# Kernel tuning notes

Measured on AMD Instinct MI355X. Metric: run time of the kernel, lower is better.

Reference implementation:

```python
import jax, jax.numpy as jnp
import numpy as np
from jax import lax

# Model hyperparameters (from module source: D_state=2, Expand=1; mamba-ssm defaults)
B_, C_, H_, W_ = 16, 128, 96, 96
D_MODEL = C_
D_INNER = 1 * D_MODEL          # expand = 1
D_STATE = 2
DT_RANK = (D_MODEL + 15) // 16  # ceil(d_model/16) = 8
D_CONV = 4
OUT_C = 128
LN_EPS = 1e-5


def setup_inputs() -> dict:
    key = jax.random.key(0)
    ks = jax.random.split(key, 10)
    s = 0.02
    x = jax.random.normal(ks[0], (B_, C_, H_, W_), dtype=jnp.float32)
    in_proj_w = jax.random.normal(ks[1], (2 * D_INNER, D_MODEL), dtype=jnp.float32) * s
    conv_w = jax.random.normal(ks[2], (D_INNER, 1, D_CONV), dtype=jnp.float32) * s
    conv_b = jnp.zeros((D_INNER,), dtype=jnp.float32)
    x_proj_w = jax.random.normal(ks[3], (DT_RANK + 2 * D_STATE, D_INNER), dtype=jnp.float32) * s
    dt_proj_w = jax.random.normal(ks[4], (D_INNER, DT_RANK), dtype=jnp.float32) * s
    # softplus^{-1}(0.01) so initial dt ~ 0.01 (standard mamba init)
    dt_proj_b = jnp.full((D_INNER,), float(np.log(np.expm1(0.01))), dtype=jnp.float32)
    A_log = jnp.log(jnp.broadcast_to(jnp.arange(1, D_STATE + 1, dtype=jnp.float32), (D_INNER, D_STATE)))
    D_param = jnp.ones((D_INNER,), dtype=jnp.float32)
    out_proj_w = jax.random.normal(ks[5], (OUT_C, D_INNER), dtype=jnp.float32) * s
    ln_gamma = jnp.ones((OUT_C,), dtype=jnp.float32)
    ln_beta = jnp.zeros((OUT_C,), dtype=jnp.float32)
    return {
        "x": x, "in_proj_w": in_proj_w, "conv_w": conv_w, "conv_b": conv_b,
        "x_proj_w": x_proj_w, "dt_proj_w": dt_proj_w, "dt_proj_b": dt_proj_b,
        "A_log": A_log, "D_param": D_param, "out_proj_w": out_proj_w,
        "ln_gamma": ln_gamma, "ln_beta": ln_beta,
    }


def _ssm_cha(x, in_proj_w, conv_w, conv_b, x_proj_w, dt_proj_w, dt_proj_b,
             A_log, D_param, out_proj_w, ln_gamma, ln_beta):
    b, c, h, w = x.shape
    L = h * w
    tokens = x.transpose(0, 2, 3, 1).reshape(b, L, c)  # [b, L, d_model]

    # in_proj -> (x_in, z)
    xz = jnp.einsum("bld,ed->ble", tokens, in_proj_w)  # [b, L, 2*d_inner]
    x_in, z = jnp.split(xz, 2, axis=-1)

    # causal depthwise conv1d over L, then SiLU
    xc = x_in.transpose(0, 2, 1)  # [b, d_inner, L]
    xc = lax.conv_general_dilated(
        xc, conv_w, window_strides=(1,), padding=[(D_CONV - 1, 0)],
        dimension_numbers=("NCH", "OIH", "NCH"), feature_group_count=D_INNER,
    ) + conv_b[None, :, None]
    x_in = jax.nn.silu(xc).transpose(0, 2, 1)  # [b, L, d_inner]

    # x_proj -> (dt, B, C)
    x_dbl = jnp.einsum("bld,ed->ble", x_in, x_proj_w)
    dt = x_dbl[..., :DT_RANK]
    Bc = x_dbl[..., DT_RANK:DT_RANK + D_STATE]         # [b, L, n]
    Cc = x_dbl[..., DT_RANK + D_STATE:]                # [b, L, n]
    dt = jax.nn.softplus(jnp.einsum("blr,dr->bld", dt, dt_proj_w) + dt_proj_b)

    # selective scan (diagonal A) via associative scan over L
    A = -jnp.exp(A_log)                                # [d_inner, n]
    dA = jnp.exp(dt[..., None] * A)                    # [b, L, d_inner, n]
    dBx = dt[..., None] * Bc[:, :, None, :] * x_in[..., None]

    def combine(e1, e2):
        a1, b1 = e1
        a2, b2 = e2
        return a1 * a2, a2 * b1 + b2

    _, hstate = lax.associative_scan(combine, (dA, dBx), axis=1)  # [b, L, d, n]
    y = jnp.sum(hstate * Cc[:, :, None, :], axis=-1) + D_param * x_in  # [b, L, d]

    y = y * jax.nn.silu(z)
    out = jnp.einsum("bld,od->blo", y, out_proj_w)     # [b, L, out_c]

    # LayerNorm over out_c
    mu = jnp.mean(out, axis=-1, keepdims=True)
    var = jnp.mean(jnp.square(out - mu), axis=-1, keepdims=True)
    out = (out - mu) * lax.rsqrt(var + LN_EPS) * ln_gamma + ln_beta

    return out.reshape(b, h, w, OUT_C).transpose(0, 3, 1, 2)


def reference(x, in_proj_w, conv_w, conv_b, x_proj_w, dt_proj_w, dt_proj_b,
              A_log, D_param, out_proj_w, ln_gamma, ln_beta):
    return _ssm_cha(x, in_proj_w, conv_w, conv_b, x_proj_w, dt_proj_w, dt_proj_b,
                    A_log, D_param, out_proj_w, ln_gamma, ln_beta)
```

## Files before the change

kernel.cpp:

```cpp
#include <hip/hip_runtime.h>
#include <hip/hip_bf16.h>

#define B_N 16
#define L_N 9216
#define LT64 144

typedef __attribute__((ext_vector_type(8))) short short8;
typedef __attribute__((ext_vector_type(4))) float floatx4;

__device__ __forceinline__ float bfu(unsigned short u) {
  return __uint_as_float(((unsigned int)u) << 16);
}
__device__ __forceinline__ unsigned short fbf(float f) {
  __hip_bfloat16 h = __float2bfloat16(f);
  return *(unsigned short*)&h;
}

__global__ __launch_bounds__(256) void k_prep(const float* __restrict__ w1,
                                              const float* __restrict__ w2,
                                              __hip_bfloat16* __restrict__ w1bt,
                                              __hip_bfloat16* __restrict__ w2bt) {
  int i = blockIdx.x * 256 + threadIdx.x;
  if (i < 256 * 128) w1bt[i] = __float2bfloat16(w1[i]);
  if (i < 128 * 128) w2bt[i] = __float2bfloat16(w2[i]);
}

__global__ __launch_bounds__(512, 4) void k_inproj_conv(
    const float* __restrict__ x, const __hip_bfloat16* __restrict__ w1bt,
    const float* __restrict__ cw, const float* __restrict__ cb,
    const float* __restrict__ xpw,
    __hip_bfloat16* __restrict__ xinb, __hip_bfloat16* __restrict__ zb,
    float* __restrict__ xdblT) {
  __shared__ __align__(16) char smem1[16384];
  __shared__ __align__(16) char smem2[34816];
  unsigned short* xs = (unsigned short*)smem1;
  unsigned short* xe = (unsigned short*)smem2;
  float (*cvs)[68] = (float(*)[68])smem2;
  float (*red)[12][64] = (float(*)[12][64])smem2;

  int blk = blockIdx.x, b = blk / LT64, lt = blk % LT64, l0 = lt * 64;
  int t = threadIdx.x;
  int lane = t & 63, wv = t >> 6;
  int col = lane & 15, quad = lane >> 4;

  const float* xb = x + (size_t)b * 128 * L_N + l0 - 16;
#pragma unroll
  for (int i = 0; i < 5; ++i) {
    int idx = t + i * 512;
    int c = idx & 127, q = idx >> 7;
    float4 v = {0.f, 0.f, 0.f, 0.f};
    if (!(lt == 0 && q < 4)) v = *(const float4*)(xb + (size_t)c * L_N + q * 4);
    int ch = c >> 3, ce = c & 7;
    if (q < 4) {
#pragma unroll
      for (int j = 0; j < 4; ++j) {
        int l = q * 4 + j;
        xe[l * 128 + (((ch ^ (l & 7)) << 3) | ce)] = fbf(((const float*)&v)[j]);
      }
    } else {
#pragma unroll
      for (int j = 0; j < 4; ++j) {
        int l = q * 4 - 16 + j;
        xs[l * 128 + (((ch ^ (l & 7)) << 3) | ce)] = fbf(((const float*)&v)[j]);
      }
    }
  }

  int e0 = wv * 32;
  const __hip_bfloat16* wbp = w1bt + (size_t)(e0 + col) * 128 + quad * 8;
  floatx4 vzero = {0.f, 0.f, 0.f, 0.f};
  floatx4 acc[2][5];
#pragma unroll
  for (int mi = 0; mi < 2; ++mi)
#pragma unroll
    for (int ni = 0; ni < 5; ++ni) acc[mi][ni] = vzero;
  short8 a0 = *(const short8*)(wbp);
  short8 a1 = *(const short8*)(wbp + 16 * 128);
  __syncthreads();

#pragma unroll
  for (int ks = 0; ks < 4; ++ks) {
    short8 n0, n1;
    if (ks < 3) {
      n0 = *(const short8*)(wbp + (ks + 1) * 32);
      n1 = *(const short8*)(wbp + 16 * 128 + (ks + 1) * 32);
    }
    short8 bfr[5];
    bfr[0] = *(const short8*)&xe[col * 128 + (((ks * 4 + quad) ^ (col & 7)) << 3)];
#pragma unroll
    for (int ni = 1; ni < 5; ++ni) {
      int row = (ni - 1) * 16 + col;
      bfr[ni] = *(const short8*)&xs[row * 128 + (((ks * 4 + quad) ^ (row & 7)) << 3)];
    }
#pragma unroll
    for (int ni = 0; ni < 5; ++ni) {
      acc[0][ni] = __builtin_amdgcn_mfma_f32_16x16x32_bf16(a0, bfr[ni], acc[0][ni], 0, 0, 0);
      acc[1][ni] = __builtin_amdgcn_mfma_f32_16x16x32_bf16(a1, bfr[ni], acc[1][ni], 0, 0, 0);
    }
    a0 = n0; a1 = n1;
  }
  __syncthreads();

  if (wv >= 4) {
    __hip_bfloat16* zbase = zb + ((size_t)b * 128 + (e0 - 128)) * L_N + l0;
#pragma unroll
    for (int mi = 0; mi < 2; ++mi)
#pragma unroll
      for (int r = 0; r < 4; ++r) {
        int dr = mi * 16 + quad * 4 + r;
#pragma unroll
        for (int ni = 1; ni < 5; ++ni)
          zbase[(size_t)dr * L_N + (ni - 1) * 16 + col] = __float2bfloat16(acc[mi][ni][r]);
      }
  } else {
#pragma unroll
    for (int mi = 0; mi < 2; ++mi)
#pragma unroll
      for (int r = 0; r < 4; ++r) {
        int d = e0 + mi * 16 + quad * 4 + r;
        if (col >= 13) cvs[d][col - 13] = acc[mi][0][r];
#pragma unroll
        for (int ni = 1; ni < 5; ++ni) cvs[d][3 + (ni - 1) * 16 + col] = acc[mi][ni][r];
      }
  }
  __syncthreads();

  float part[12];
#pragma unroll
  for (int m = 0; m < 12; ++m) part[m] = 0.f;
  for (int dd = 0; dd < 16; ++dd) {
    int d = wv * 16 + dd;
    float v = cb[d] + cw[d * 4 + 0] * cvs[d][lane] + cw[d * 4 + 1] * cvs[d][lane + 1]
                    + cw[d * 4 + 2] * cvs[d][lane + 2] + cw[d * 4 + 3] * cvs[d][lane + 3];
    v = v / (1.f + __expf(-v));
    xinb[((size_t)b * 128 + d) * L_N + l0 + lane] = __float2bfloat16(v);
#pragma unroll
    for (int m = 0; m < 12; ++m) part[m] += xpw[m * 128 + d] * v;
  }
  __syncthreads();
#pragma unroll
  for (int m = 0; m < 12; ++m) red[wv][m][lane] = part[m];
  __syncthreads();
  for (int idx = t; idx < 12 * 64; idx += 512) {
    int m = idx >> 6, l = idx & 63;
    float s = 0.f;
#pragma unroll
    for (int w8 = 0; w8 < 8; ++w8) s += red[w8][m][l];
    xdblT[((size_t)b * 12 + m) * L_N + l0 + l] = s;
  }
}

__global__ __launch_bounds__(256) void k_scan(
    const float* __restrict__ xdblT, const float* __restrict__ dtw,
    const float* __restrict__ dtb, const float* __restrict__ alog,
    const float* __restrict__ dpar,
    const __hip_bfloat16* __restrict__ xinb, const __hip_bfloat16* __restrict__ zb,
    __hip_bfloat16* __restrict__ yb) {
  __shared__ float agg[2][4][4];
  __shared__ float carry[2][2];
  int blk = blockIdx.x, b = blk >> 7, d = blk & 127;
  int t = threadIdx.x, lane = t & 63, wv = t >> 6;
  float A0 = -__expf(alog[2 * d]), A1 = -__expf(alog[2 * d + 1]);
  float Dv = dpar[d], dtbv = dtb[d];
  float w[8];
#pragma unroll
  for (int i = 0; i < 8; ++i) w[i] = dtw[d * 8 + i];
  if (t == 0) { carry[0][0] = 0.f; carry[0][1] = 0.f; }
  __syncthreads();
  const float* xdT = xdblT + (size_t)b * 12 * L_N;
  const unsigned short* xi = (const unsigned short*)xinb + ((size_t)b * 128 + d) * L_N;
  const unsigned short* zr = (const unsigned short*)zb + ((size_t)b * 128 + d) * L_N;
  unsigned short* yo = (unsigned short*)yb + ((size_t)b * 128 + d) * L_N;
  for (int it = 0; it < 9; ++it) {
    int p = it & 1;
    int lb = it * 1024 + t * 4;
    float4 q[12];
#pragma unroll
    for (int m = 0; m < 12; ++m) q[m] = *(const float4*)(xdT + (size_t)m * L_N + lb);
    ushort4 xu = *(const ushort4*)(xi + lb);
    ushort4 zu = *(const ushort4*)(zr + lb);
    float xv[4] = {bfu(xu.x), bfu(xu.y), bfu(xu.z), bfu(xu.w)};
    float zv[4] = {bfu(zu.x), bfu(zu.y), bfu(zu.z), bfu(zu.w)};
    float A0p[4], X0p[4], A1p[4], X1p[4];
#pragma unroll
    for (int j = 0; j < 4; ++j) {
      float dtp = dtbv;
#pragma unroll
      for (int m = 0; m < 8; ++m) dtp += w[m] * ((const float*)&q[m])[j];
      float dt = (dtp > 15.f) ? dtp : __logf(1.f + __expf(dtp));
      float a0 = __expf(dt * A0), a1 = __expf(dt * A1);
      float dtx = dt * xv[j];
      float x0 = dtx * ((const float*)&q[8])[j];
      float x1 = dtx * ((const float*)&q[9])[j];
      if (j == 0) { A0p[0] = a0; X0p[0] = x0; A1p[0] = a1; X1p[0] = x1; }
      else {
        A0p[j] = a0 * A0p[j - 1]; X0p[j] = a0 * X0p[j - 1] + x0;
        A1p[j] = a1 * A1p[j - 1]; X1p[j] = a1 * X1p[j - 1] + x1;
      }
    }
    float wA0 = A0p[3], wX0 = X0p[3], wA1 = A1p[3], wX1 = X1p[3];
#pragma unroll
    for (int off = 1; off < 64; off <<= 1) {
      float pA0 = __shfl_up(wA0, off, 64), pX0 = __shfl_up(wX0, off, 64);
      float pA1 = __shfl_up(wA1, off, 64), pX1 = __shfl_up(wX1, off, 64);
      if (lane >= off) {
        wX0 += wA0 * pX0; wA0 *= pA0;
        wX1 += wA1 * pX1; wA1 *= pA1;
      }
    }
    if (lane == 63) { agg[p][wv][0] = wA0; agg[p][wv][1] = wX0; agg[p][wv][2] = wA1; agg[p][wv][3] = wX1; }
    float eA0 = __shfl_up(wA0, 1, 64), eX0 = __shfl_up(wX0, 1, 64);
    float eA1 = __shfl_up(wA1, 1, 64), eX1 = __shfl_up(wX1, 1, 64);
    if (lane == 0) { eA0 = 1.f; eX0 = 0.f; eA1 = 1.f; eX1 = 0.f; }
    __syncthreads();
    float h0 = carry[p][0], h1 = carry[p][1];
    for (int jw = 0; jw < wv; ++jw) {
      h0 = agg[p][jw][0] * h0 + agg[p][jw][1];
      h1 = agg[p][jw][2] * h1 + agg[p][jw][3];
    }
    h0 = eA0 * h0 + eX0;
    h1 = eA1 * h1 + eX1;
    if (t == 255) {
      carry[p ^ 1][0] = A0p[3] * h0 + X0p[3];
      carry[p ^ 1][1] = A1p[3] * h1 + X1p[3];
    }
    ushort4 yu;
    unsigned short* yp = (unsigned short*)&yu;
#pragma unroll
    for (int j = 0; j < 4; ++j) {
      float hh0 = A0p[j] * h0 + X0p[j];
      float hh1 = A1p[j] * h1 + X1p[j];
      float y = hh0 * ((const float*)&q[10])[j] + hh1 * ((const float*)&q[11])[j] + Dv * xv[j];
      y *= zv[j] / (1.f + __expf(-zv[j]));
      yp[j] = fbf(y);
    }
    *(ushort4*)(yo + lb) = yu;
  }
}

__global__ __launch_bounds__(256) void k_outln(
    const __hip_bfloat16* __restrict__ yb, const __hip_bfloat16* __restrict__ w2bt,
    const float* __restrict__ gam, const float* __restrict__ bet,
    float* __restrict__ out) {
  __shared__ unsigned short yts[64 * 128];
  __shared__ float red_s[4][64], red_q[4][64];
  __shared__ float gs[128], bs[128];
  int blk = blockIdx.x, b = blk / LT64, lt = blk % LT64, l0 = lt * 64;
  int t = threadIdx.x;
  if (t < 128) { gs[t] = gam[t]; bs[t] = bet[t]; }
  const unsigned short* ybb = (const unsigned short*)yb + (size_t)b * 128 * L_N + l0;
#pragma unroll
  for (int i = 0; i < 8; ++i) {
    int idx = t + i * 256;
    int dd = idx >> 4, l4 = (idx & 15) * 4;
    ushort4 v = *(const ushort4*)(ybb + (size_t)dd * L_N + l4);
    int ch = dd >> 3, ce = dd & 7;
    yts[(l4 + 0) * 128 + (((ch ^ ((l4 + 0) & 7)) << 3) | ce)] = v.x;
    yts[(l4 + 1) * 128 + (((ch ^ ((l4 + 1) & 7)) << 3) | ce)] = v.y;
    yts[(l4 + 2) * 128 + (((ch ^ ((l4 + 2) & 7)) << 3) | ce)] = v.z;
    yts[(l4 + 3) * 128 + (((ch ^ ((l4 + 3) & 7)) << 3) | ce)] = v.w;
  }
  int lane = t & 63, wv = t >> 6;
  int col = lane & 15, quad = lane >> 4;
  int o0 = wv * 32;
  short8 afr[2][4];
#pragma unroll
  for (int mi = 0; mi < 2; ++mi)
#pragma unroll
    for (int ks = 0; ks < 4; ++ks)
      afr[mi][ks] = *(const short8*)(w2bt + (size_t)(o0 + mi * 16 + col) * 128 + ks * 32 + quad * 8);
  floatx4 vzero = {0.f, 0.f, 0.f, 0.f};
  floatx4 acc[2][4];
#pragma unroll
  for (int mi = 0; mi < 2; ++mi)
#pragma unroll
    for (int ni = 0; ni < 4; ++ni) acc[mi][ni] = vzero;
  __syncthreads();
#pragma unroll
  for (int ks = 0; ks < 4; ++ks) {
    short8 bfr[4];
#pragma unroll
    for (int ni = 0; ni < 4; ++ni) {
      int row = ni * 16 + col;
      bfr[ni] = *(const short8*)&yts[row * 128 + (((ks * 4 + quad) ^ (row & 7)) << 3)];
    }
#pragma unroll
    for (int mi = 0; mi < 2; ++mi)
#pragma unroll
      for (int ni = 0; ni < 4; ++ni)
        acc[mi][ni] = __builtin_amdgcn_mfma_f32_16x16x32_bf16(afr[mi][ks], bfr[ni], acc[mi][ni], 0, 0, 0);
  }
  float s[4], q[4];
#pragma unroll
  for (int ni = 0; ni < 4; ++ni) {
    float ss = 0.f, qq = 0.f;
#pragma unroll
    for (int mi = 0; mi < 2; ++mi)
#pragma unroll
      for (int r = 0; r < 4; ++r) {
        float v = acc[mi][ni][r];
        ss += v; qq += v * v;
      }
    ss += __shfl_xor(ss, 16, 64); ss += __shfl_xor(ss, 32, 64);
    qq += __shfl_xor(qq, 16, 64); qq += __shfl_xor(qq, 32, 64);
    s[ni] = ss; q[ni] = qq;
  }
  if (quad == 0) {
#pragma unroll
    for (int ni = 0; ni < 4; ++ni) {
      red_s[wv][ni * 16 + col] = s[ni];
      red_q[wv][ni * 16 + col] = q[ni];
    }
  }
  __syncthreads();
  float mu[4], rstd[4];
#pragma unroll
  for (int ni = 0; ni < 4; ++ni) {
    int li = ni * 16 + col;
    float ts = red_s[0][li] + red_s[1][li] + red_s[2][li] + red_s[3][li];
    float tq = red_q[0][li] + red_q[1][li] + red_q[2][li] + red_q[3][li];
    float m = ts * (1.f / 128.f);
    float var = tq * (1.f / 128.f) - m * m;
    mu[ni] = m;
    rstd[ni] = rsqrtf(var + 1e-5f);
  }
  float* ob = out + (size_t)b * 128 * L_N;
#pragma unroll
  for (int mi = 0; mi < 2; ++mi)
#pragma unroll
    for (int r = 0; r < 4; ++r) {
      int o = o0 + mi * 16 + quad * 4 + r;
      float g = gs[o], bb = bs[o];
#pragma unroll
      for (int ni = 0; ni < 4; ++ni)
        ob[(size_t)o * L_N + l0 + ni * 16 + col] = (acc[mi][ni][r] - mu[ni]) * rstd[ni] * g + bb;
    }
}

extern "C" void kernel_launch(void* const* d_in, const int* in_sizes, int n_in,
                              void* d_out, int out_size, void* d_ws, size_t ws_size,
                              hipStream_t stream) {
  const float* x    = (const float*)d_in[0];
  const float* w1   = (const float*)d_in[1];
  const float* cw   = (const float*)d_in[2];
  const float* cb   = (const float*)d_in[3];
  const float* xpw  = (const float*)d_in[4];
  const float* dtw  = (const float*)d_in[5];
  const float* dtb  = (const float*)d_in[6];
  const float* alog = (const float*)d_in[7];
  const float* dpar = (const float*)d_in[8];
  const float* w2   = (const float*)d_in[9];
  const float* gam  = (const float*)d_in[10];
  const float* bet  = (const float*)d_in[11];
  float* out = (float*)d_out;

  float* ws = (float*)d_ws;
  const size_t NBL = (size_t)B_N * 128 * L_N;
  float* xdblT = ws;
  __hip_bfloat16* xinb = (__hip_bfloat16*)(ws + (size_t)B_N * 12 * L_N);
  __hip_bfloat16* zb   = xinb + NBL;
  __hip_bfloat16* yb   = zb + NBL;
  __hip_bfloat16* w1bt = yb + NBL;
  __hip_bfloat16* w2bt = w1bt + 256 * 128;

  k_prep<<<128, 256, 0, stream>>>(w1, w2, w1bt, w2bt);
  k_inproj_conv<<<B_N * LT64, 512, 0, stream>>>(x, w1bt, cw, cb, xpw, xinb, zb, xdblT);
  k_scan<<<B_N * 128, 256, 0, stream>>>(xdblT, dtw, dtb, alog, dpar, xinb, zb, yb);
  k_outln<<<B_N * LT64, 256, 0, stream>>>(yb, w2bt, gam, bet, out);
}
```

Baseline: 291.5 us.

## Process three L-tiles per block in inproj_conv, reusing the halo from the previous tile

Each in-projection/conv block now loops over three consecutive 64-token tiles instead of one. The last 16 rows of the previous tile's staged input serve as the conv halo, so the overlapping 16-token reload is skipped, and the next tile's load is issued before the conv/SiLU/x_proj phase. The conv staging buffer is also stored as fp16 instead of fp32, and the cross-wave reduction is halved to four slots to cut shared memory. The risk is fewer blocks (768 vs 2304) and thus less parallelism, plus a small loss of precision in the fp16 pre-conv values.

```diff
diff --git a/kernel.cpp b/kernel.cpp
--- a/kernel.cpp
+++ b/kernel.cpp
@@ -1,5 +1,6 @@
 #include <hip/hip_runtime.h>
 #include <hip/hip_bf16.h>
+#include <hip/hip_fp16.h>
 
 #define B_N 16
 #define L_N 9216
@@ -14,6 +15,14 @@
 __device__ __forceinline__ unsigned short fbf(float f) {
   __hip_bfloat16 h = __float2bfloat16(f);
   return *(unsigned short*)&h;
+}
+__device__ __forceinline__ unsigned short fh(float f) {
+  __half h = __float2half(f);
+  return *(unsigned short*)&h;
+}
+__device__ __forceinline__ float hfu(unsigned short u) {
+  __half h = *(__half*)&u;
+  return __half2float(h);
 }
 
 __global__ __launch_bounds__(256) void k_prep(const float* __restrict__ w1,
@@ -31,122 +40,153 @@
     const float* __restrict__ xpw,
     __hip_bfloat16* __restrict__ xinb, __hip_bfloat16* __restrict__ zb,
     float* __restrict__ xdblT) {
-  __shared__ __align__(16) char smem1[16384];
-  __shared__ __align__(16) char smem2[34816];
-  unsigned short* xs = (unsigned short*)smem1;
+  __shared__ __align__(16) unsigned short Xb[2][64 * 128];
+  __shared__ __align__(16) char smem2[18432];
   unsigned short* xe = (unsigned short*)smem2;
-  float (*cvs)[68] = (float(*)[68])smem2;
-  float (*red)[12][64] = (float(*)[12][64])smem2;
-
-  int blk = blockIdx.x, b = blk / LT64, lt = blk % LT64, l0 = lt * 64;
+  unsigned short (*cvs)[72] = (unsigned short(*)[72])smem2;
+  float (*red4)[12][64] = (float(*)[12][64])smem2;
+
+  int blk = blockIdx.x, b = blk / 48, g = blk % 48;
   int t = threadIdx.x;
   int lane = t & 63, wv = t >> 6;
   int col = lane & 15, quad = lane >> 4;
-
-  const float* xb = x + (size_t)b * 128 * L_N + l0 - 16;
-#pragma unroll
-  for (int i = 0; i < 5; ++i) {
-    int idx = t + i * 512;
-    int c = idx & 127, q = idx >> 7;
-    float4 v = {0.f, 0.f, 0.f, 0.f};
-    if (!(lt == 0 && q < 4)) v = *(const float4*)(xb + (size_t)c * L_N + q * 4);
-    int ch = c >> 3, ce = c & 7;
-    if (q < 4) {
-#pragma unroll
-      for (int j = 0; j < 4; ++j) {
-        int l = q * 4 + j;
-        xe[l * 128 + (((ch ^ (l & 7)) << 3) | ce)] = fbf(((const float*)&v)[j]);
-      }
-    } else {
-#pragma unroll
-      for (int j = 0; j < 4; ++j) {
-        int l = q * 4 - 16 + j;
-        xs[l * 128 + (((ch ^ (l & 7)) << 3) | ce)] = fbf(((const float*)&v)[j]);
-      }
-    }
-  }
-
   int e0 = wv * 32;
   const __hip_bfloat16* wbp = w1bt + (size_t)(e0 + col) * 128 + quad * 8;
-  floatx4 vzero = {0.f, 0.f, 0.f, 0.f};
-  floatx4 acc[2][5];
-#pragma unroll
-  for (int mi = 0; mi < 2; ++mi)
-#pragma unroll
-    for (int ni = 0; ni < 5; ++ni) acc[mi][ni] = vzero;
-  short8 a0 = *(const short8*)(wbp);
-  short8 a1 = *(const short8*)(wbp + 16 * 128);
-  __syncthreads();
-
-#pragma unroll
-  for (int ks = 0; ks < 4; ++ks) {
-    short8 n0, n1;
-    if (ks < 3) {
-      n0 = *(const short8*)(wbp + (ks + 1) * 32);
-      n1 = *(const short8*)(wbp + 16 * 128 + (ks + 1) * 32);
-    }
-    short8 bfr[5];
-    bfr[0] = *(const short8*)&xe[col * 128 + (((ks * 4 + quad) ^ (col & 7)) << 3)];
-#pragma unroll
-    for (int ni = 1; ni < 5; ++ni) {
-      int row = (ni - 1) * 16 + col;
-      bfr[ni] = *(const short8*)&xs[row * 128 + (((ks * 4 + quad) ^ (row & 7)) << 3)];
-    }
-#pragma unroll
-    for (int ni = 0; ni < 5; ++ni) {
-      acc[0][ni] = __builtin_amdgcn_mfma_f32_16x16x32_bf16(a0, bfr[ni], acc[0][ni], 0, 0, 0);
-      acc[1][ni] = __builtin_amdgcn_mfma_f32_16x16x32_bf16(a1, bfr[ni], acc[1][ni], 0, 0, 0);
-    }
-    a0 = n0; a1 = n1;
-  }
-  __syncthreads();
-
-  if (wv >= 4) {
-    __hip_bfloat16* zbase = zb + ((size_t)b * 128 + (e0 - 128)) * L_N + l0;
+
+  {
+    int lt = g * 3, l0 = lt * 64;
+    const float* xsrc = x + (size_t)b * 128 * L_N + l0 - 16;
+#pragma unroll
+    for (int i = 0; i < 5; ++i) {
+      int idx = t + i * 512;
+      int c = idx & 127, q = idx >> 7;
+      float4 v = {0.f, 0.f, 0.f, 0.f};
+      if (!(lt == 0 && q < 4)) v = *(const float4*)(xsrc + (size_t)c * L_N + q * 4);
+      int ch = c >> 3, ce = c & 7;
+      if (q < 4) {
+#pragma unroll
+        for (int j = 0; j < 4; ++j) {
+          int l = q * 4 + j;
+          xe[l * 128 + (((ch ^ (l & 7)) << 3) | ce)] = fbf(((const float*)&v)[j]);
+        }
+      } else {
+#pragma unroll
+        for (int j = 0; j < 4; ++j) {
+          int l = q * 4 - 16 + j;
+          Xb[0][l * 128 + (((ch ^ (l & 7)) << 3) | ce)] = fbf(((const float*)&v)[j]);
+        }
+      }
+    }
+  }
+
+  for (int s = 0; s < 3; ++s) {
+    int lt = g * 3 + s, l0 = lt * 64;
+    unsigned short* Xc = Xb[s & 1];
+    const unsigned short* bnd = (s == 0) ? xe : &Xb[(s ^ 1) & 1][48 * 128];
+
+    floatx4 vzero = {0.f, 0.f, 0.f, 0.f};
+    floatx4 acc[2][5];
 #pragma unroll
     for (int mi = 0; mi < 2; ++mi)
 #pragma unroll
-      for (int r = 0; r < 4; ++r) {
-        int dr = mi * 16 + quad * 4 + r;
-#pragma unroll
-        for (int ni = 1; ni < 5; ++ni)
-          zbase[(size_t)dr * L_N + (ni - 1) * 16 + col] = __float2bfloat16(acc[mi][ni][r]);
-      }
-  } else {
-#pragma unroll
-    for (int mi = 0; mi < 2; ++mi)
-#pragma unroll
-      for (int r = 0; r < 4; ++r) {
-        int d = e0 + mi * 16 + quad * 4 + r;
-        if (col >= 13) cvs[d][col - 13] = acc[mi][0][r];
-#pragma unroll
-        for (int ni = 1; ni < 5; ++ni) cvs[d][3 + (ni - 1) * 16 + col] = acc[mi][ni][r];
-      }
-  }
-  __syncthreads();
-
-  float part[12];
-#pragma unroll
-  for (int m = 0; m < 12; ++m) part[m] = 0.f;
-  for (int dd = 0; dd < 16; ++dd) {
-    int d = wv * 16 + dd;
-    float v = cb[d] + cw[d * 4 + 0] * cvs[d][lane] + cw[d * 4 + 1] * cvs[d][lane + 1]
-                    + cw[d * 4 + 2] * cvs[d][lane + 2] + cw[d * 4 + 3] * cvs[d][lane + 3];
-    v = v / (1.f + __expf(-v));
-    xinb[((size_t)b * 128 + d) * L_N + l0 + lane] = __float2bfloat16(v);
-#pragma unroll
-    for (int m = 0; m < 12; ++m) part[m] += xpw[m * 128 + d] * v;
-  }
-  __syncthreads();
-#pragma unroll
-  for (int m = 0; m < 12; ++m) red[wv][m][lane] = part[m];
-  __syncthreads();
-  for (int idx = t; idx < 12 * 64; idx += 512) {
-    int m = idx >> 6, l = idx & 63;
-    float s = 0.f;
-#pragma unroll
-    for (int w8 = 0; w8 < 8; ++w8) s += red[w8][m][l];
-    xdblT[((size_t)b * 12 + m) * L_N + l0 + l] = s;
+      for (int ni = 0; ni < 5; ++ni) acc[mi][ni] = vzero;
+    short8 a0 = *(const short8*)(wbp);
+    short8 a1 = *(const short8*)(wbp + 16 * 128);
+    __syncthreads();
+
+#pragma unroll
+    for (int ks = 0; ks < 4; ++ks) {
+      short8 n0, n1;
+      if (ks < 3) {
+        n0 = *(const short8*)(wbp + (ks + 1) * 32);
+        n1 = *(const short8*)(wbp + 16 * 128 + (ks + 1) * 32);
+      }
+      short8 bfr[5];
+      bfr[0] = *(const short8*)&bnd[col * 128 + (((ks * 4 + quad) ^ (col & 7)) << 3)];
+#pragma unroll
+      for (int ni = 1; ni < 5; ++ni) {
+        int row = (ni - 1) * 16 + col;
+        bfr[ni] = *(const short8*)&Xc[row * 128 + (((ks * 4 + quad) ^ (row & 7)) << 3)];
+      }
+#pragma unroll
+      for (int ni = 0; ni < 5; ++ni) {
+        acc[0][ni] = __builtin_amdgcn_mfma_f32_16x16x32_bf16(a0, bfr[ni], acc[0][ni], 0, 0, 0);
+        acc[1][ni] = __builtin_amdgcn_mfma_f32_16x16x32_bf16(a1, bfr[ni], acc[1][ni], 0, 0, 0);
+      }
+      a0 = n0; a1 = n1;
+    }
+    __syncthreads();
+
+    if (wv >= 4) {
+      __hip_bfloat16* zbase = zb + ((size_t)b * 128 + (e0 - 128)) * L_N + l0;
+#pragma unroll
+      for (int mi = 0; mi < 2; ++mi)
+#pragma unroll
+        for (int r = 0; r < 4; ++r) {
+          int dr = mi * 16 + quad * 4 + r;
+#pragma unroll
+          for (int ni = 1; ni < 5; ++ni)
+            zbase[(size_t)dr * L_N + (ni - 1) * 16 + col] = __float2bfloat16(acc[mi][ni][r]);
+        }
+    } else {
+#pragma unroll
+      for (int mi = 0; mi < 2; ++mi)
+#pragma unroll
+        for (int r = 0; r < 4; ++r) {
+          int d = e0 + mi * 16 + quad * 4 + r;
+          if (col >= 13) cvs[d][col - 13] = fh(acc[mi][0][r]);
+#pragma unroll
+          for (int ni = 1; ni < 5; ++ni) cvs[d][3 + (ni - 1) * 16 + col] = fh(acc[mi][ni][r]);
+        }
+    }
+    __syncthreads();
+
+    if (s < 2) {
+      const float* xsrc = x + (size_t)b * 128 * L_N + (size_t)(lt + 1) * 64;
+      unsigned short* Xn = Xb[(s + 1) & 1];
+#pragma unroll
+      for (int i = 0; i < 4; ++i) {
+        int idx = t + i * 512;
+        int c = idx & 127, q = idx >> 7;
+        float4 v = *(const float4*)(xsrc + (size_t)c * L_N + q * 4);
+        int ch = c >> 3, ce = c & 7;
+#pragma unroll
+        for (int j = 0; j < 4; ++j) {
+          int l = q * 4 + j;
+          Xn[l * 128 + (((ch ^ (l & 7)) << 3) | ce)] = fbf(((const float*)&v)[j]);
+        }
+      }
+    }
+
+    float part[12];
+#pragma unroll
+    for (int m = 0; m < 12; ++m) part[m] = 0.f;
+    for (int dd = 0; dd < 16; ++dd) {
+      int d = wv * 16 + dd;
+      float v = cb[d] + cw[d * 4 + 0] * hfu(cvs[d][lane]) + cw[d * 4 + 1] * hfu(cvs[d][lane + 1])
+                      + cw[d * 4 + 2] * hfu(cvs[d][lane + 2]) + cw[d * 4 + 3] * hfu(cvs[d][lane + 3]);
+      v = v / (1.f + __expf(-v));
+      xinb[((size_t)b * 128 + d) * L_N + l0 + lane] = __float2bfloat16(v);
+#pragma unroll
+      for (int m = 0; m < 12; ++m) part[m] += xpw[m * 128 + d] * v;
+    }
+    __syncthreads();
+
+    if (wv < 4) {
+#pragma unroll
+      for (int m = 0; m < 12; ++m) red4[wv][m][lane] = part[m];
+    }
+    __syncthreads();
+    if (wv >= 4) {
+#pragma unroll
+      for (int m = 0; m < 12; ++m) red4[wv - 4][m][lane] += part[m];
+    }
+    __syncthreads();
+    for (int idx = t; idx < 12 * 64; idx += 512) {
+      int m = idx >> 6, l = idx & 63;
+      float ssum = red4[0][m][l] + red4[1][m][l] + red4[2][m][l] + red4[3][m][l];
+      xdblT[((size_t)b * 12 + m) * L_N + l0 + l] = ssum;
+    }
   }
 }
 
@@ -364,7 +404,7 @@
   __hip_bfloat16* w2bt = w1bt + 256 * 128;
 
   k_prep<<<128, 256, 0, stream>>>(w1, w2, w1bt, w2bt);
-  k_inproj_conv<<<B_N * LT64, 512, 0, stream>>>(x, w1bt, cw, cb, xpw, xinb, zb, xdblT);
+  k_inproj_conv<<<B_N * 48, 512, 0, stream>>>(x, w1bt, cw, cb, xpw, xinb, zb, xdblT);
   k_scan<<<B_N * 128, 256, 0, stream>>>(xdblT, dtw, dtb, alog, dpar, xinb, zb, yb);
   k_outln<<<B_N * LT64, 256, 0, stream>>>(yb, w2bt, gam, bet, out);
 }
```

After: 361.3 us. 1.24x slower.
